# Kernel optimization log

Measured on AMD Instinct MI355X. Metric: run time of the kernel, lower is better.

Reference implementation:

```python
import jax, jax.numpy as jnp
import numpy as np

N = 50000
NEG_SLOPE = 0.2


def _gat_layer(x, src, dst, W, a_src, a_dst, b, heads, out_ch, concat):
    # x: [N, F_in]; W: [F_in, heads*out_ch]; a_src/a_dst: [heads, out_ch]; b: bias
    h = (x @ W).reshape(N, heads, out_ch)                      # [N,H,C]
    s_src = jnp.einsum('nhc,hc->nh', h, a_src)                 # [N,H]
    s_dst = jnp.einsum('nhc,hc->nh', h, a_dst)                 # [N,H]
    e = jax.nn.leaky_relu(s_src[src] + s_dst[dst], NEG_SLOPE)  # [E,H]
    # segment softmax over edges sharing the same destination node
    m = jax.ops.segment_max(e, dst, num_segments=N)
    m = jax.lax.stop_gradient(jnp.where(jnp.isfinite(m), m, 0.0))
    w = jnp.exp(e - m[dst])
    denom = jax.ops.segment_sum(w, dst, num_segments=N)
    alpha = w / (denom[dst] + 1e-16)                           # [E,H]
    out = jax.ops.segment_sum(alpha[:, :, None] * h[src], dst, num_segments=N)  # [N,H,C]
    out = out.reshape(N, heads * out_ch) if concat else out.mean(axis=1)
    return out + b


def setup_inputs() -> dict:
    key = jax.random.key(0)
    ks = jax.random.split(key, 16)
    F_in, Hd, H1, H3, F_out = 128, 64, 4, 6, 64
    E = 800000
    x = jax.random.normal(ks[0], (N, F_in), dtype=jnp.float32)
    edge_index = jax.random.randint(ks[1], (2, E), 0, N, dtype=jnp.int64)

    def glorot(k, shape, fan_in):
        return jax.random.normal(k, shape, dtype=jnp.float32) * (1.0 / np.sqrt(fan_in))

    params = {
        'W1': glorot(ks[2], (F_in, H1 * Hd), F_in),
        'a1_src': glorot(ks[3], (H1, Hd), Hd),
        'a1_dst': glorot(ks[4], (H1, Hd), Hd),
        'b1': jnp.zeros((H1 * Hd,), dtype=jnp.float32),
        'W2': glorot(ks[5], (H1 * Hd, H1 * Hd), H1 * Hd),
        'a2_src': glorot(ks[6], (H1, Hd), Hd),
        'a2_dst': glorot(ks[7], (H1, Hd), Hd),
        'b2': jnp.zeros((H1 * Hd,), dtype=jnp.float32),
        'W3': glorot(ks[8], (H1 * Hd, H3 * F_out), H1 * Hd),
        'a3_src': glorot(ks[9], (H3, F_out), F_out),
        'a3_dst': glorot(ks[10], (H3, F_out), F_out),
        'b3': jnp.zeros((F_out,), dtype=jnp.float32),
    }
    return {'x': x, 'edge_index': edge_index, **params}


def reference(x, edge_index, W1, a1_src, a1_dst, b1, W2, a2_src, a2_dst, b2, W3, a3_src, a3_dst, b3):
    # PyG GATConv default add_self_loops=True
    loops = jnp.arange(N, dtype=edge_index.dtype)
    src = jnp.concatenate([edge_index[0], loops])
    dst = jnp.concatenate([edge_index[1], loops])
    x1 = jax.nn.elu(_gat_layer(x, src, dst, W1, a1_src, a1_dst, b1, heads=4, out_ch=64, concat=True))
    x2 = jax.nn.elu(_gat_layer(x1, src, dst, W2, a2_src, a2_dst, b2, heads=4, out_ch=64, concat=True))
    x3 = _gat_layer(x2, src, dst, W3, a3_src, a3_dst, b3, heads=6, out_ch=64, concat=False)
    return x3
```

## Files before the change

### kernel.cpp

```cpp
#include <hip/hip_runtime.h>
#include <hip/hip_bf16.h>
#include <hip/hip_fp16.h>
#include <math.h>

#define NNODES 50000

typedef __attribute__((ext_vector_type(8))) short short8v;
typedef __attribute__((ext_vector_type(4))) float f32x4;
typedef unsigned short ushort_t;
typedef unsigned int uint_t;

__device__ inline ushort_t f2bf_bits(float v) {
    union { __hip_bfloat16 b; ushort_t u; } c;
    c.b = __float2bfloat16(v);
    return c.u;
}
__device__ inline float bfbits2f(ushort_t u) {
    union { __hip_bfloat16 b; ushort_t u; } c;
    c.u = u;
    return __bfloat162float(c.b);
}
__device__ inline ushort_t f2h_bits(float v) {
    union { __half h; ushort_t u; } c;
    c.h = __float2half(v);
    return c.u;
}
__device__ inline void cvt2(uint_t u, float& a, float& b) {
    union { uint_t u; __half2 h; } c; c.u = u;
    a = __low2float(c.h); b = __high2float(c.h);
}
__device__ inline uint_t fmap(float f) {
    uint_t b = __float_as_uint(f);
    return (b & 0x80000000u) ? ~b : (b | 0x80000000u);
}
__device__ inline float funmap(uint_t u) {
    return __uint_as_float((u & 0x80000000u) ? (u & 0x7FFFFFFFu) : ~u);
}

__global__ __launch_bounds__(256)
void split_kernel(const float4* __restrict__ in, ushort4* __restrict__ hi,
                  ushort4* __restrict__ lo, int n4) {
    int i = blockIdx.x * blockDim.x + threadIdx.x;
    if (i >= n4) return;
    float4 v = in[i];
    ushort4 h, l;
    h.x = f2bf_bits(v.x); l.x = f2bf_bits(v.x - bfbits2f(h.x));
    h.y = f2bf_bits(v.y); l.y = f2bf_bits(v.y - bfbits2f(h.y));
    h.z = f2bf_bits(v.z); l.z = f2bf_bits(v.z - bfbits2f(h.z));
    h.w = f2bf_bits(v.w); l.w = f2bf_bits(v.w - bfbits2f(h.w));
    hi[i] = h; lo[i] = l;
}

__global__ __launch_bounds__(256)
void wprep_all(const float* __restrict__ W1, const float* __restrict__ W2,
               const float* __restrict__ W3,
               ushort_t* __restrict__ w1h, ushort_t* __restrict__ w1l,
               ushort_t* __restrict__ w2h, ushort_t* __restrict__ w2l,
               ushort_t* __restrict__ w3h, ushort_t* __restrict__ w3l) {
    int idx = blockIdx.x * blockDim.x + threadIdx.x;
    const float* W; ushort_t* hT; ushort_t* lT; int K, N;
    if (idx < 128 * 256) { W = W1; hT = w1h; lT = w1l; K = 128; N = 256; }
    else if (idx < 128 * 256 + 256 * 256) {
        idx -= 128 * 256; W = W2; hT = w2h; lT = w2l; K = 256; N = 256;
    } else {
        idx -= 128 * 256 + 256 * 256;
        if (idx >= 256 * 384) return;
        W = W3; hT = w3h; lT = w3l; K = 256; N = 384;
    }
    int k = idx / N, n = idx - k * N;
    float v = W[idx];
    ushort_t hb = f2bf_bits(v);
    hT[(size_t)n * K + k] = hb;
    lT[(size_t)n * K + k] = f2bf_bits(v - bfbits2f(hb));
}

template<int H>
__global__ __launch_bounds__(256)
void gemm_fused(const ushort_t* __restrict__ Ahi, const ushort_t* __restrict__ Alo,
                const ushort_t* __restrict__ Bhi, const ushort_t* __restrict__ Blo,
                ushort_t* __restrict__ h16, float* __restrict__ ssrc,
                float* __restrict__ sdst, uint_t* __restrict__ gmaxu,
                const float* __restrict__ a_src, const float* __restrict__ a_dst,
                int M, int K) {
    __shared__ char smem[24576];
    __shared__ float sSs[64][2], sDs[64][2];
    __shared__ uint_t gblk[2];

    const int tid = threadIdx.x;
    const int lane = tid & 63;
    const int wid = tid >> 6;
    const int wm = wid >> 1, wn = wid & 1;
    const int bm = blockIdx.y * 64;
    const int bn = blockIdx.x * 128;
    const int r15 = lane & 15;
    const int g4 = lane >> 4;

    if (tid < 128) { ((float*)sSs)[tid] = 0.f; ((float*)sDs)[tid] = 0.f; }
    if (tid < 2) gblk[tid] = 0;

    char* As_hi = smem;
    char* As_lo = smem + 4096;
    char* Bs_hi = smem + 8192;
    char* Bs_lo = smem + 16384;

    const int srow = tid >> 2;
    const int skc  = tid & 3;
    const size_t arow  = (size_t)(bm + srow) * K;
    const size_t brow0 = (size_t)(bn + srow) * K;
    const size_t brow1 = (size_t)(bn + 64 + srow) * K;

    f32x4 acc[2][4] = {};

    for (int k0 = 0; k0 < K; k0 += 32) {
        short8v a0 = *(const short8v*)&Ahi[arow  + k0 + skc * 8];
        short8v l0 = *(const short8v*)&Alo[arow  + k0 + skc * 8];
        short8v b0 = *(const short8v*)&Bhi[brow0 + k0 + skc * 8];
        short8v b1 = *(const short8v*)&Bhi[brow1 + k0 + skc * 8];
        short8v m0 = *(const short8v*)&Blo[brow0 + k0 + skc * 8];
        short8v m1 = *(const short8v*)&Blo[brow1 + k0 + skc * 8];
        __syncthreads();
        *(short8v*)(As_hi + skc * 1024 + srow * 16)        = a0;
        *(short8v*)(As_lo + skc * 1024 + srow * 16)        = l0;
        *(short8v*)(Bs_hi + skc * 2048 + srow * 16)        = b0;
        *(short8v*)(Bs_hi + skc * 2048 + (64 + srow) * 16) = b1;
        *(short8v*)(Bs_lo + skc * 2048 + srow * 16)        = m0;
        *(short8v*)(Bs_lo + skc * 2048 + (64 + srow) * 16) = m1;
        __syncthreads();

        short8v ah[2], al[2], bh[4], bl[4];
        #pragma unroll
        for (int mi = 0; mi < 2; ++mi) {
            int row = wm * 32 + mi * 16 + r15;
            ah[mi] = *(const short8v*)(As_hi + g4 * 1024 + row * 16);
            al[mi] = *(const short8v*)(As_lo + g4 * 1024 + row * 16);
        }
        #pragma unroll
        for (int nj = 0; nj < 4; ++nj) {
            int row = wn * 64 + nj * 16 + r15;
            bh[nj] = *(const short8v*)(Bs_hi + g4 * 2048 + row * 16);
            bl[nj] = *(const short8v*)(Bs_lo + g4 * 2048 + row * 16);
        }
        #pragma unroll
        for (int mi = 0; mi < 2; ++mi)
            #pragma unroll
            for (int nj = 0; nj < 4; ++nj) {
                acc[mi][nj] = __builtin_amdgcn_mfma_f32_16x16x32_bf16(ah[mi], bh[nj], acc[mi][nj], 0, 0, 0);
                acc[mi][nj] = __builtin_amdgcn_mfma_f32_16x16x32_bf16(ah[mi], bl[nj], acc[mi][nj], 0, 0, 0);
                acc[mi][nj] = __builtin_amdgcn_mfma_f32_16x16x32_bf16(al[mi], bh[nj], acc[mi][nj], 0, 0, 0);
            }
    }
    __syncthreads();

    ushort_t* h2 = (ushort_t*)smem;
    const int headg = (bn >> 6) + wn;
    float asv[4], adv[4];
    #pragma unroll
    for (int nj = 0; nj < 4; ++nj) {
        asv[nj] = a_src[headg * 64 + nj * 16 + r15];
        adv[nj] = a_dst[headg * 64 + nj * 16 + r15];
    }
    #pragma unroll
    for (int mi = 0; mi < 2; ++mi) {
        #pragma unroll
        for (int reg = 0; reg < 4; ++reg) {
            int row_l = wm * 32 + mi * 16 + g4 * 4 + reg;
            int csw = ((row_l >> 2) & 3) << 2;
            float pS = 0.f, pD = 0.f;
            #pragma unroll
            for (int nj = 0; nj < 4; ++nj) {
                float v = acc[mi][nj][reg];
                int col_l = wn * 64 + nj * 16 + r15;
                h2[row_l * 128 + (col_l ^ csw)] = f2h_bits(v);
                pS += v * asv[nj];
                pD += v * adv[nj];
            }
            #pragma unroll
            for (int off = 1; off < 16; off <<= 1) {
                pS += __shfl_xor(pS, off);
                pD += __shfl_xor(pD, off);
            }
            if (r15 == 0) {
                sSs[row_l][wn] = pS;
                sDs[row_l][wn] = pD;
            }
        }
    }
    __syncthreads();

    uint_t* plane = (uint_t*)h16 + (size_t)(bn >> 7) * ((size_t)NNODES * 64);
    for (int u = tid; u < 64 * 64; u += 256) {
        int n_l = u >> 6, c = u & 63;
        if (bm + n_l < M) {
            int csw = ((n_l >> 2) & 3) << 2;
            uint_t lo = h2[n_l * 128 + (c ^ csw)];
            uint_t hi = h2[n_l * 128 + 64 + (c ^ csw)];
            plane[(size_t)(bm + n_l) * 64 + c] = lo | (hi << 16);
        }
    }
    if (tid < 128) {
        int row = tid >> 1, hl = tid & 1;
        if (bm + row < M) {
            int hg = (bn >> 6) + hl;
            float vS = sSs[row][hl];
            ssrc[(size_t)(bm + row) * H + hg] = vS;
            sdst[(size_t)(bm + row) * H + hg] = sDs[row][hl];
            atomicMax(&gblk[hl], fmap(vS));
        }
    }
    __syncthreads();
    if (tid < 2) atomicMax(&gmaxu[(bn >> 6) + tid], gblk[tid]);
}

__global__ void deg_kernel(const int* __restrict__ ei, int E, int Nn,
                           int* __restrict__ deg) {
    int e = blockIdx.x * blockDim.x + threadIdx.x;
    int tot = E + Nn;
    if (e >= tot) return;
    int d = (e < E) ? ei[E + e] : (e - E);
    atomicAdd(&deg[d], 1);
}

__global__ __launch_bounds__(1024)
void scan1_kernel(const int* __restrict__ deg, int* __restrict__ offs,
                  int* __restrict__ bsum, int n) {
    __shared__ int sh[1024];
    int t = threadIdx.x;
    int i = blockIdx.x * 1024 + t;
    int v = (i < n) ? deg[i] : 0;
    sh[t] = v;
    __syncthreads();
    for (int off = 1; off < 1024; off <<= 1) {
        int add = (t >= off) ? sh[t - off] : 0;
        __syncthreads();
        sh[t] += add;
        __syncthreads();
    }
    if (i < n) offs[i + 1] = sh[t];
    if (t == 1023) bsum[blockIdx.x] = sh[1023];
}

__global__ __launch_bounds__(64)
void scan2_kernel(const int* __restrict__ bsum, int* __restrict__ bexcl, int nb) {
    int t = threadIdx.x;
    int v = (t < nb) ? bsum[t] : 0;
    int orig = v;
    #pragma unroll
    for (int off = 1; off < 64; off <<= 1) {
        int u = __shfl_up(v, off);
        if (t >= off) v += u;
    }
    if (t < nb) bexcl[t] = v - orig;
}

__global__ void scan3_kernel(const int* __restrict__ deg, int* __restrict__ offs,
                             const int* __restrict__ bexcl, int* __restrict__ cursor,
                             int n) {
    int i = blockIdx.x * blockDim.x + threadIdx.x;
    if (i == 0) offs[0] = 0;
    if (i < n) {
        int inc = offs[i + 1] + bexcl[i >> 10];
        offs[i + 1] = inc;
        cursor[i] = inc - deg[i];
    }
}

__global__ void scatter_kernel(const int* __restrict__ ei, int E, int Nn,
                               int* __restrict__ cursor, int* __restrict__ csr_src) {
    int e = blockIdx.x * blockDim.x + threadIdx.x;
    int tot = E + Nn;
    if (e >= tot) return;
    int s, d;
    if (e < E) { s = ei[e]; d = ei[E + e]; }
    else       { s = d = e - E; }
    int pos = atomicAdd(&cursor[d], 1);
    csr_src[pos] = s;
}

template<int H>
__device__ inline void loadS(const float* __restrict__ p, float* v) {
    if constexpr (H == 4) {
        float4 t = *(const float4*)p;
        v[0] = t.x; v[1] = t.y; v[2] = t.z; v[3] = t.w;
    } else {
        const float2* q = (const float2*)p;
        float2 a = q[0], b = q[1], c = q[2];
        v[0] = a.x; v[1] = a.y; v[2] = b.x; v[3] = b.y; v[4] = c.x; v[5] = c.y;
    }
}

template<int H>
__global__ __launch_bounds__(256)
void smw_kernel(const float* __restrict__ ssrc, const float* __restrict__ sdst,
                const uint_t* __restrict__ gmaxu, const int* __restrict__ offs,
                const int* __restrict__ csr, float* __restrict__ wbuf,
                float* __restrict__ rden, int Nn) {
    int wid = (blockIdx.x * blockDim.x + threadIdx.x) >> 6;
    int lane = threadIdx.x & 63;
    if (wid >= Nn) return;
    int beg = offs[wid], end = offs[wid + 1];
    float sd[H], mx[H], den[H];
    #pragma unroll
    for (int h = 0; h < H; ++h) {
        sd[h] = sdst[wid * H + h];
        float t = funmap(gmaxu[h]) + sd[h];
        mx[h] = t > 0.f ? t : 0.2f * t;
        den[h] = 0.f;
    }
    for (int i = beg + lane; i < end; i += 64) {
        int s = csr[i];
        float sv[H];
        loadS<H>(ssrc + (size_t)s * H, sv);
        #pragma unroll
        for (int h = 0; h < H; ++h) {
            float sc = sv[h] + sd[h];
            sc = sc > 0.f ? sc : 0.2f * sc;
            float w = __expf(sc - mx[h]);
            wbuf[(size_t)i * H + h] = w;
            den[h] += w;
        }
    }
    #pragma unroll
    for (int h = 0; h < H; ++h) {
        #pragma unroll
        for (int off = 32; off; off >>= 1) den[h] += __shfl_xor(den[h], off);
    }
    if (lane == 0) {
        #pragma unroll
        for (int h = 0; h < H; ++h) rden[wid * H + h] = 1.f / (den[h] + 1e-16f);
    }
}

template<int H, bool MEAN>
__global__ __launch_bounds__(256)
void agg_kernel(const ushort_t* __restrict__ h16, const float* __restrict__ wbuf,
                const float* __restrict__ rden, const int* __restrict__ offs,
                const int* __restrict__ csr, const float* __restrict__ bias,
                float* __restrict__ outf, ushort_t* __restrict__ ohi,
                ushort_t* __restrict__ olo, int Nn) {
    constexpr int P = H / 2;
    int wid = (blockIdx.x * blockDim.x + threadIdx.x) >> 6;
    int lane = threadIdx.x & 63;
    if (wid >= Nn) return;
    int beg = offs[wid], end = offs[wid + 1];
    const uint_t* up = (const uint_t*)h16;
    const size_t psz = (size_t)Nn * 64;

    constexpr int U = (H == 4) ? 8 : 4;
    float acc0[H] = {}, acc1[H] = {};
    int i = beg;
    for (; i + U <= end; i += U) {
        int s[U];
        #pragma unroll
        for (int j = 0; j < U; ++j) s[j] = csr[i + j];
        uint_t g[U][P];
        #pragma unroll
        for (int j = 0; j < U; ++j)
            #pragma unroll
            for (int p = 0; p < P; ++p)
                g[j][p] = up[(size_t)p * psz + (size_t)s[j] * 64 + lane];
        float w[U][H];
        #pragma unroll
        for (int j = 0; j < U; ++j) {
            if constexpr (H == 4) {
                float4 t = *(const float4*)&wbuf[(size_t)(i + j) * 4];
                w[j][0] = t.x; w[j][1] = t.y; w[j][2] = t.z; w[j][3] = t.w;
            } else {
                const float2* q = (const float2*)&wbuf[(size_t)(i + j) * 6];
                float2 a = q[0], b = q[1], c = q[2];
                w[j][0] = a.x; w[j][1] = a.y; w[j][2] = b.x;
                w[j][3] = b.y; w[j][4] = c.x; w[j][5] = c.y;
            }
        }
        #pragma unroll
        for (int j = 0; j < U; ++j) {
            float v[H];
            #pragma unroll
            for (int p = 0; p < P; ++p) cvt2(g[j][p], v[2 * p], v[2 * p + 1]);
            float* a = (j & 1) ? acc1 : acc0;
            #pragma unroll
            for (int h = 0; h < H; ++h) a[h] += w[j][h] * v[h];
        }
    }
    for (; i < end; ++i) {
        int s = csr[i];
        float v[H];
        #pragma unroll
        for (int p = 0; p < P; ++p) {
            uint_t g = up[(size_t)p * psz + (size_t)s * 64 + lane];
            cvt2(g, v[2 * p], v[2 * p + 1]);
        }
        #pragma unroll
        for (int h = 0; h < H; ++h) acc0[h] += wbuf[(size_t)i * H + h] * v[h];
    }

    if (!MEAN) {
        #pragma unroll
        for (int h = 0; h < H; ++h) {
            float val = (acc0[h] + acc1[h]) * rden[wid * H + h] + bias[h * 64 + lane];
            val = val > 0.f ? val : expm1f(val);
            size_t idx = (size_t)wid * (H * 64) + h * 64 + lane;
            ushort_t hb = f2bf_bits(val);
            ohi[idx] = hb;
            olo[idx] = f2bf_bits(val - bfbits2f(hb));
        }
    } else {
        float m = 0.f;
        #pragma unroll
        for (int h = 0; h < H; ++h) m += (acc0[h] + acc1[h]) * rden[wid * H + h];
        outf[(size_t)wid * 64 + lane] = m * (1.f / (float)H) + bias[lane];
    }
}

extern "C" void kernel_launch(void* const* d_in, const int* in_sizes, int n_in,
                              void* d_out, int out_size, void* d_ws, size_t ws_size,
                              hipStream_t stream) {
    const float* x     = (const float*)d_in[0];
    const int*   ei    = (const int*)d_in[1];
    const float* W1    = (const float*)d_in[2];
    const float* a1s   = (const float*)d_in[3];
    const float* a1d   = (const float*)d_in[4];
    const float* b1    = (const float*)d_in[5];
    const float* W2    = (const float*)d_in[6];
    const float* a2s   = (const float*)d_in[7];
    const float* a2d   = (const float*)d_in[8];
    const float* b2    = (const float*)d_in[9];
    const float* W3    = (const float*)d_in[10];
    const float* a3s   = (const float*)d_in[11];
    const float* a3d   = (const float*)d_in[12];
    const float* b3    = (const float*)d_in[13];
    float* out = (float*)d_out;

    const int Nn = NNODES;
    const int E  = in_sizes[1] / 2;
    const int Etot = E + Nn;

    char* p = (char*)d_ws;
    auto carve = [&](size_t bytes) {
        char* r = p;
        p += (bytes + 255) & ~(size_t)255;
        return (void*)r;
    };
    ushort_t* h16   = (ushort_t*)carve((size_t)Nn * 384 * 2);
    ushort_t* R1    = (ushort_t*)carve((size_t)Nn * 256 * 4);
    ushort_t* x_hi  = R1;
    ushort_t* x_lo  = R1 + (size_t)Nn * 128;
    ushort_t* x1_hi = R1;
    ushort_t* x1_lo = R1 + (size_t)Nn * 256;
    ushort_t* w1hi  = (ushort_t*)carve((size_t)128 * 256 * 2);
    ushort_t* w1lo  = (ushort_t*)carve((size_t)128 * 256 * 2);
    ushort_t* w2hi  = (ushort_t*)carve((size_t)256 * 256 * 2);
    ushort_t* w2lo  = (ushort_t*)carve((size_t)256 * 256 * 2);
    ushort_t* w3hi  = (ushort_t*)carve((size_t)256 * 384 * 2);
    ushort_t* w3lo  = (ushort_t*)carve((size_t)256 * 384 * 2);
    float* ssrc   = (float*)carve((size_t)Nn * 6 * 4);
    float* sdst   = (float*)carve((size_t)Nn * 6 * 4);
    float* rden   = (float*)carve((size_t)Nn * 6 * 4);
    float* wbuf   = (float*)carve((size_t)Etot * 6 * 4);
    int*   deg    = (int*)carve((size_t)Nn * 4);
    int*   offs   = (int*)carve((size_t)(Nn + 1) * 4);
    int*   cursor = (int*)carve((size_t)Nn * 4);
    int*   csr    = (int*)carve((size_t)Etot * 4);
    uint_t* gmaxu = (uint_t*)carve(18 * 4);
    int*   bsum   = (int*)carve(64 * 4);
    int*   bexcl  = (int*)carve(64 * 4);

    hipMemsetAsync(deg, 0, (size_t)Nn * 4, stream);
    hipMemsetAsync(gmaxu, 0, 18 * 4, stream);
    {
        int nb = (Etot + 255) / 256;
        int nsb = (Nn + 1023) / 1024;
        deg_kernel<<<nb, 256, 0, stream>>>(ei, E, Nn, deg);
        scan1_kernel<<<nsb, 1024, 0, stream>>>(deg, offs, bsum, Nn);
        scan2_kernel<<<1, 64, 0, stream>>>(bsum, bexcl, nsb);
        scan3_kernel<<<(Nn + 255) / 256, 256, 0, stream>>>(deg, offs, bexcl, cursor, Nn);
        scatter_kernel<<<nb, 256, 0, stream>>>(ei, E, Nn, cursor, csr);
    }

    {
        int n4 = Nn * 128 / 4;
        split_kernel<<<(n4 + 255) / 256, 256, 0, stream>>>(
            (const float4*)x, (ushort4*)x_hi, (ushort4*)x_lo, n4);
        int wtot = 128 * 256 + 256 * 256 + 256 * 384;
        wprep_all<<<(wtot + 255) / 256, 256, 0, stream>>>(W1, W2, W3, w1hi, w1lo,
                                                          w2hi, w2lo, w3hi, w3lo);
    }

    const int node_blocks = (Nn + 3) / 4;
    const int gemm_rows = (Nn + 63) / 64;

    {
        dim3 g(2, gemm_rows);
        gemm_fused<4><<<g, 256, 0, stream>>>(x_hi, x_lo, w1hi, w1lo, h16,
                                             ssrc, sdst, gmaxu + 0, a1s, a1d, Nn, 128);
        smw_kernel<4><<<node_blocks, 256, 0, stream>>>(ssrc, sdst, gmaxu + 0, offs, csr,
                                                       wbuf, rden, Nn);
        agg_kernel<4, false><<<node_blocks, 256, 0, stream>>>(h16, wbuf, rden, offs, csr, b1,
                                                              nullptr, x1_hi, x1_lo, Nn);
    }
    {
        dim3 g(2, gemm_rows);
        gemm_fused<4><<<g, 256, 0, stream>>>(x1_hi, x1_lo, w2hi, w2lo, h16,
                                             ssrc, sdst, gmaxu + 6, a2s, a2d, Nn, 256);
        smw_kernel<4><<<node_blocks, 256, 0, stream>>>(ssrc, sdst, gmaxu + 6, offs, csr,
                                                       wbuf, rden, Nn);
        agg_kernel<4, false><<<node_blocks, 256, 0, stream>>>(h16, wbuf, rden, offs, csr, b2,
                                                              nullptr, x1_hi, x1_lo, Nn);
    }
    {
        dim3 g(3, gemm_rows);
        gemm_fused<6><<<g, 256, 0, stream>>>(x1_hi, x1_lo, w3hi, w3lo, h16,
                                             ssrc, sdst, gmaxu + 12, a3s, a3d, Nn, 256);
        smw_kernel<6><<<node_blocks, 256, 0, stream>>>(ssrc, sdst, gmaxu + 12, offs, csr,
                                                       wbuf, rden, Nn);
        agg_kernel<6, true><<<node_blocks, 256, 0, stream>>>(h16, wbuf, rden, offs, csr, b3,
                                                             out, nullptr, nullptr, Nn);
    }
}
```

Measured before the change: 564.0 us.

## Fuse softmax weight computation into aggregation kernel, removing edge weight buffer

Merges the per-edge softmax-weight kernel into the aggregation kernel. Each wavefront now computes weights for a 64-edge chunk in registers and broadcasts them and the source indices with shuffles instead of writing and rereading an edge weight buffer and reciprocal denominators. This removes one launch per layer and the global-memory round trip for the edge weights. In exchange, each chunk adds a dependent score load before the feature gathers, plus extra shuffle traffic.

```diff
diff --git a/kernel.cpp b/kernel.cpp
--- a/kernel.cpp
+++ b/kernel.cpp
@@ -288,16 +288,22 @@
     }
 }
 
-template<int H>
+template<int H, bool MEAN>
 __global__ __launch_bounds__(256)
-void smw_kernel(const float* __restrict__ ssrc, const float* __restrict__ sdst,
-                const uint_t* __restrict__ gmaxu, const int* __restrict__ offs,
-                const int* __restrict__ csr, float* __restrict__ wbuf,
-                float* __restrict__ rden, int Nn) {
+void agg_kernel(const ushort_t* __restrict__ h16, const float* __restrict__ ssrc,
+                const float* __restrict__ sdst, const uint_t* __restrict__ gmaxu,
+                const int* __restrict__ offs, const int* __restrict__ csr,
+                const float* __restrict__ bias, float* __restrict__ outf,
+                ushort_t* __restrict__ ohi, ushort_t* __restrict__ olo, int Nn) {
+    constexpr int P = H / 2;
+    constexpr int U = (H == 4) ? 8 : 4;
     int wid = (blockIdx.x * blockDim.x + threadIdx.x) >> 6;
     int lane = threadIdx.x & 63;
     if (wid >= Nn) return;
     int beg = offs[wid], end = offs[wid + 1];
+    const uint_t* up = (const uint_t*)h16;
+    const size_t psz = (size_t)Nn * 64;
+
     float sd[H], mx[H], den[H];
     #pragma unroll
     for (int h = 0; h < H; ++h) {
@@ -306,97 +312,76 @@
         mx[h] = t > 0.f ? t : 0.2f * t;
         den[h] = 0.f;
     }
-    for (int i = beg + lane; i < end; i += 64) {
-        int s = csr[i];
-        float sv[H];
-        loadS<H>(ssrc + (size_t)s * H, sv);
-        #pragma unroll
-        for (int h = 0; h < H; ++h) {
-            float sc = sv[h] + sd[h];
-            sc = sc > 0.f ? sc : 0.2f * sc;
-            float w = __expf(sc - mx[h]);
-            wbuf[(size_t)i * H + h] = w;
-            den[h] += w;
-        }
-    }
+
+    float acc0[H] = {}, acc1[H] = {};
+    for (int cbeg = beg; cbeg < end; cbeg += 64) {
+        int cdeg = end - cbeg; if (cdeg > 64) cdeg = 64;
+        float wreg[H];
+        int sreg = 0;
+        #pragma unroll
+        for (int h = 0; h < H; ++h) wreg[h] = 0.f;
+        if (lane < cdeg) {
+            sreg = csr[cbeg + lane];
+            float sv[H];
+            loadS<H>(ssrc + (size_t)sreg * H, sv);
+            #pragma unroll
+            for (int h = 0; h < H; ++h) {
+                float sc = sv[h] + sd[h];
+                sc = sc > 0.f ? sc : 0.2f * sc;
+                float w = __expf(sc - mx[h]);
+                wreg[h] = w;
+                den[h] += w;
+            }
+        }
+        int i = 0;
+        for (; i + U <= cdeg; i += U) {
+            int s[U];
+            #pragma unroll
+            for (int j = 0; j < U; ++j) s[j] = __shfl(sreg, i + j);
+            uint_t g[U][P];
+            #pragma unroll
+            for (int j = 0; j < U; ++j)
+                #pragma unroll
+                for (int p = 0; p < P; ++p)
+                    g[j][p] = up[(size_t)p * psz + (size_t)s[j] * 64 + lane];
+            float w[U][H];
+            #pragma unroll
+            for (int j = 0; j < U; ++j)
+                #pragma unroll
+                for (int h = 0; h < H; ++h) w[j][h] = __shfl(wreg[h], i + j);
+            #pragma unroll
+            for (int j = 0; j < U; ++j) {
+                float v[H];
+                #pragma unroll
+                for (int p = 0; p < P; ++p) cvt2(g[j][p], v[2 * p], v[2 * p + 1]);
+                float* a = (j & 1) ? acc1 : acc0;
+                #pragma unroll
+                for (int h = 0; h < H; ++h) a[h] += w[j][h] * v[h];
+            }
+        }
+        for (; i < cdeg; ++i) {
+            int s = __shfl(sreg, i);
+            float v[H];
+            #pragma unroll
+            for (int p = 0; p < P; ++p) {
+                uint_t g = up[(size_t)p * psz + (size_t)s * 64 + lane];
+                cvt2(g, v[2 * p], v[2 * p + 1]);
+            }
+            #pragma unroll
+            for (int h = 0; h < H; ++h) acc0[h] += __shfl(wreg[h], i) * v[h];
+        }
+    }
+
     #pragma unroll
     for (int h = 0; h < H; ++h) {
         #pragma unroll
         for (int off = 32; off; off >>= 1) den[h] += __shfl_xor(den[h], off);
     }
-    if (lane == 0) {
-        #pragma unroll
-        for (int h = 0; h < H; ++h) rden[wid * H + h] = 1.f / (den[h] + 1e-16f);
-    }
-}
-
-template<int H, bool MEAN>
-__global__ __launch_bounds__(256)
-void agg_kernel(const ushort_t* __restrict__ h16, const float* __restrict__ wbuf,
-                const float* __restrict__ rden, const int* __restrict__ offs,
-                const int* __restrict__ csr, const float* __restrict__ bias,
-                float* __restrict__ outf, ushort_t* __restrict__ ohi,
-                ushort_t* __restrict__ olo, int Nn) {
-    constexpr int P = H / 2;
-    int wid = (blockIdx.x * blockDim.x + threadIdx.x) >> 6;
-    int lane = threadIdx.x & 63;
-    if (wid >= Nn) return;
-    int beg = offs[wid], end = offs[wid + 1];
-    const uint_t* up = (const uint_t*)h16;
-    const size_t psz = (size_t)Nn * 64;
-
-    constexpr int U = (H == 4) ? 8 : 4;
-    float acc0[H] = {}, acc1[H] = {};
-    int i = beg;
-    for (; i + U <= end; i += U) {
-        int s[U];
-        #pragma unroll
-        for (int j = 0; j < U; ++j) s[j] = csr[i + j];
-        uint_t g[U][P];
-        #pragma unroll
-        for (int j = 0; j < U; ++j)
-            #pragma unroll
-            for (int p = 0; p < P; ++p)
-                g[j][p] = up[(size_t)p * psz + (size_t)s[j] * 64 + lane];
-        float w[U][H];
-        #pragma unroll
-        for (int j = 0; j < U; ++j) {
-            if constexpr (H == 4) {
-                float4 t = *(const float4*)&wbuf[(size_t)(i + j) * 4];
-                w[j][0] = t.x; w[j][1] = t.y; w[j][2] = t.z; w[j][3] = t.w;
-            } else {
-                const float2* q = (const float2*)&wbuf[(size_t)(i + j) * 6];
-                float2 a = q[0], b = q[1], c = q[2];
-                w[j][0] = a.x; w[j][1] = a.y; w[j][2] = b.x;
-                w[j][3] = b.y; w[j][4] = c.x; w[j][5] = c.y;
-            }
-        }
-        #pragma unroll
-        for (int j = 0; j < U; ++j) {
-            float v[H];
-            #pragma unroll
-            for (int p = 0; p < P; ++p) cvt2(g[j][p], v[2 * p], v[2 * p + 1]);
-            float* a = (j & 1) ? acc1 : acc0;
-            #pragma unroll
-            for (int h = 0; h < H; ++h) a[h] += w[j][h] * v[h];
-        }
-    }
-    for (; i < end; ++i) {
-        int s = csr[i];
-        float v[H];
-        #pragma unroll
-        for (int p = 0; p < P; ++p) {
-            uint_t g = up[(size_t)p * psz + (size_t)s * 64 + lane];
-            cvt2(g, v[2 * p], v[2 * p + 1]);
-        }
-        #pragma unroll
-        for (int h = 0; h < H; ++h) acc0[h] += wbuf[(size_t)i * H + h] * v[h];
-    }
 
     if (!MEAN) {
         #pragma unroll
         for (int h = 0; h < H; ++h) {
-            float val = (acc0[h] + acc1[h]) * rden[wid * H + h] + bias[h * 64 + lane];
+            float val = (acc0[h] + acc1[h]) / (den[h] + 1e-16f) + bias[h * 64 + lane];
             val = val > 0.f ? val : expm1f(val);
             size_t idx = (size_t)wid * (H * 64) + h * 64 + lane;
             ushort_t hb = f2bf_bits(val);
@@ -406,7 +391,8 @@
     } else {
         float m = 0.f;
         #pragma unroll
-        for (int h = 0; h < H; ++h) m += (acc0[h] + acc1[h]) * rden[wid * H + h];
+        for (int h = 0; h < H; ++h)
+            m += (acc0[h] + acc1[h]) / (den[h] + 1e-16f);
         outf[(size_t)wid * 64 + lane] = m * (1.f / (float)H) + bias[lane];
     }
 }
@@ -454,8 +440,6 @@
     ushort_t* w3lo  = (ushort_t*)carve((size_t)256 * 384 * 2);
     float* ssrc   = (float*)carve((size_t)Nn * 6 * 4);
     float* sdst   = (float*)carve((size_t)Nn * 6 * 4);
-    float* rden   = (float*)carve((size_t)Nn * 6 * 4);
-    float* wbuf   = (float*)carve((size_t)Etot * 6 * 4);
     int*   deg    = (int*)carve((size_t)Nn * 4);
     int*   offs   = (int*)carve((size_t)(Nn + 1) * 4);
     int*   cursor = (int*)carve((size_t)Nn * 4);
@@ -492,27 +476,24 @@
         dim3 g(2, gemm_rows);
         gemm_fused<4><<<g, 256, 0, stream>>>(x_hi, x_lo, w1hi, w1lo, h16,
                                              ssrc, sdst, gmaxu + 0, a1s, a1d, Nn, 128);
-        smw_kernel<4><<<node_blocks, 256, 0, stream>>>(ssrc, sdst, gmaxu + 0, offs, csr,
-                                                       wbuf, rden, Nn);
-        agg_kernel<4, false><<<node_blocks, 256, 0, stream>>>(h16, wbuf, rden, offs, csr, b1,
+        agg_kernel<4, false><<<node_blocks, 256, 0, stream>>>(h16, ssrc, sdst, gmaxu + 0,
+                                                              offs, csr, b1,
                                                               nullptr, x1_hi, x1_lo, Nn);
     }
     {
         dim3 g(2, gemm_rows);
         gemm_fused<4><<<g, 256, 0, stream>>>(x1_hi, x1_lo, w2hi, w2lo, h16,
                                              ssrc, sdst, gmaxu + 6, a2s, a2d, Nn, 256);
-        smw_kernel<4><<<node_blocks, 256, 0, stream>>>(ssrc, sdst, gmaxu + 6, offs, csr,
-                                                       wbuf, rden, Nn);
-        agg_kernel<4, false><<<node_blocks, 256, 0, stream>>>(h16, wbuf, rden, offs, csr, b2,
+        agg_kernel<4, false><<<node_blocks, 256, 0, stream>>>(h16, ssrc, sdst, gmaxu + 6,
+                                                              offs, csr, b2,
                                                               nullptr, x1_hi, x1_lo, Nn);
     }
     {
         dim3 g(3, gemm_rows);
         gemm_fused<6><<<g, 256, 0, stream>>>(x1_hi, x1_lo, w3hi, w3lo, h16,
                                              ssrc, sdst, gmaxu + 12, a3s, a3d, Nn, 256);
-        smw_kernel<6><<<node_blocks, 256, 0, stream>>>(ssrc, sdst, gmaxu + 12, offs, csr,
-                                                       wbuf, rden, Nn);
-        agg_kernel<6, true><<<node_blocks, 256, 0, stream>>>(h16, wbuf, rden, offs, csr, b3,
+        agg_kernel<6, true><<<node_blocks, 256, 0, stream>>>(h16, ssrc, sdst, gmaxu + 12,
+                                                             offs, csr, b3,
                                                              out, nullptr, nullptr, Nn);
     }
 }
```

After: 543.1 us. 3.7% less time.
